# Performance work log

Measured on AMD Instinct MI355X. Metric: run time of the kernel, lower is better.

Reference implementation:

```python
import jax, jax.numpy as jnp
import numpy as np

N = 50000        # nodes
E = 1600000      # edges
IN = 256         # in_features
AD = 128         # attention_dim
H = 8            # heads
DK = AD // H     # per-head dim


def setup_inputs() -> dict:
    key = jax.random.key(0)
    ks = jax.random.split(key, 9)
    hi = jax.random.normal(ks[0], (N, IN), jnp.float32)
    radial = jax.random.uniform(ks[1], (E, 1), jnp.float32)
    edge = jax.random.randint(ks[2], (2, E), 0, N)
    # learned params (torch Linear: y = x @ W.T + b)
    Qw = jax.random.normal(ks[3], (AD, IN), jnp.float32) * 0.05
    Qb = jax.random.normal(ks[4], (AD,), jnp.float32) * 0.05
    Qrw = jax.random.normal(ks[5], (AD, 1), jnp.float32) * 0.05
    Qrb = jax.random.normal(ks[6], (AD,), jnp.float32) * 0.05
    Kw = jax.random.normal(ks[7], (AD, IN), jnp.float32) * 0.05
    Kb = jax.random.normal(ks[8], (AD,), jnp.float32) * 0.05
    return {"hi": hi, "radial": radial, "Qw": Qw, "Qb": Qb,
            "Qrw": Qrw, "Qrb": Qrb, "Kw": Kw, "Kb": Kb, "edge": edge}


def _segment_softmax(logits, seg, num_segments):
    # numerically stable softmax grouped by segment id (per head column)
    m = jax.ops.segment_max(logits, seg, num_segments=num_segments)  # [N, H]
    ex = jnp.exp(logits - m[seg])
    s = jax.ops.segment_sum(ex, seg, num_segments=num_segments)      # [N, H]
    return ex / s[seg]


def reference(hi, radial, Qw, Qb, Qrw, Qrb, Kw, Kb, edge):
    # node projections: [N, AD] -> [N, H, DK]
    q = (hi @ Qw.T + Qb).reshape(-1, H, DK)
    k = (hi @ Kw.T + Kb).reshape(-1, H, DK)
    # per-edge radial projection: [E, AD] -> [E, H, DK]
    q_rad = (radial @ Qrw.T + Qrb).reshape(-1, H, DK)
    # gather by edge endpoints; original transposes (1,2) then sums dim=1,
    # which is exactly a contraction over DK per head.
    src = q[edge[0]] + q_rad          # [E, H, DK]
    dst_k = k[edge[1]]                # [E, H, DK]
    prods = jnp.sum(src * dst_k, axis=-1) / np.sqrt(DK)  # [E, H]
    # square_plus=False, reweight_attention=False, attention_norm_idx=0
    attention = _segment_softmax(prods, edge[0], N)
    return attention, prods
```

## Files before the change

### kernel.cpp

```cpp
#include <hip/hip_runtime.h>
#include <hip/hip_fp16.h>
#include <math.h>

#define N_NODES 50000
#define EDGES   1600000
#define IN_F    256
#define AD      128
#define H       8
#define DK      16

typedef __attribute__((ext_vector_type(8))) _Float16 half8;
typedef __attribute__((ext_vector_type(4))) _Float16 half4;
typedef __attribute__((ext_vector_type(4))) float floatx4;

#ifndef __has_builtin
#define __has_builtin(x) 0
#endif

__global__ void wswz_kernel(const float* __restrict__ Qw,
                            const float* __restrict__ Kw,
                            half8* __restrict__ Wfrag) {
    const int idx = blockIdx.x * blockDim.x + threadIdx.x;
    if (idx >= 8 * 16 * 64) return;
    const int lane = idx & 63;
    const int nb   = (idx >> 6) & 15;
    const int kb   = idx >> 10;
    const int n    = nb * 16 + (lane & 15);
    const int k0   = kb * 32 + ((lane >> 4) << 3);
    const float* row = (n < AD) ? (Qw + (size_t)n * IN_F)
                                : (Kw + (size_t)(n - AD) * IN_F);
    half8 v;
#pragma unroll
    for (int j = 0; j < 8; j++) v[j] = (_Float16)row[k0 + j];
    Wfrag[idx] = v;
}

#define APAD 264
__global__ __launch_bounds__(256) void proj_mfma_kernel(
    const float* __restrict__ hi, const half8* __restrict__ Wfrag,
    const float* __restrict__ Qb, const float* __restrict__ Kb,
    __half* __restrict__ qh, __half* __restrict__ kh)
{
    __shared__ _Float16 Atile[64][APAD];
    const int r0 = blockIdx.x * 64;
    const int t  = threadIdx.x;

    {
        const int row = t >> 2;
        const int c4  = t & 3;
        const bool valid = (r0 + row) < N_NODES;
        const float4* src = (const float4*)(hi + (size_t)(r0 + row) * IN_F);
#pragma unroll
        for (int i = 0; i < 16; i++) {
            const int col4 = c4 + i * 4;
            float4 v = valid ? src[col4] : make_float4(0.f, 0.f, 0.f, 0.f);
            half4 hv;
            hv[0] = (_Float16)v.x; hv[1] = (_Float16)v.y;
            hv[2] = (_Float16)v.z; hv[3] = (_Float16)v.w;
            *(half4*)&Atile[row][col4 * 4] = hv;
        }
    }
    __syncthreads();

    const int wave = t >> 6;
    const int lane = t & 63;
    const int m    = lane & 15;
    const int quad = lane >> 4;

    floatx4 acc[4][4];
#pragma unroll
    for (int a = 0; a < 4; a++)
#pragma unroll
        for (int b = 0; b < 4; b++) acc[a][b] = (floatx4)0.f;

#pragma unroll
    for (int kb = 0; kb < 8; kb++) {
        half8 Af[4], Bf[4];
#pragma unroll
        for (int rb = 0; rb < 4; rb++)
            Af[rb] = *(const half8*)&Atile[rb * 16 + m][kb * 32 + quad * 8];
#pragma unroll
        for (int nbi = 0; nbi < 4; nbi++)
            Bf[nbi] = Wfrag[(size_t)(kb * 16 + wave * 4 + nbi) * 64 + lane];
#pragma unroll
        for (int rb = 0; rb < 4; rb++)
#pragma unroll
            for (int nbi = 0; nbi < 4; nbi++)
                acc[rb][nbi] = __builtin_amdgcn_mfma_f32_16x16x32_f16(
                    Af[rb], Bf[nbi], acc[rb][nbi], 0, 0, 0);
    }

#pragma unroll
    for (int nbi = 0; nbi < 4; nbi++) {
        const int n   = wave * 64 + nbi * 16 + m;
        const float bias = (n < AD) ? Qb[n] : Kb[n - AD];
        __half* out   = (n < AD) ? qh : kh;
        const int ncol = n & (AD - 1);
#pragma unroll
        for (int rb = 0; rb < 4; rb++) {
#pragma unroll
            for (int reg = 0; reg < 4; reg++) {
                const int row = r0 + rb * 16 + quad * 4 + reg;
                if (row < N_NODES)
                    out[(size_t)row * AD + ncol] = __float2half(acc[rb][nbi][reg] + bias);
            }
        }
    }
}

__global__ __launch_bounds__(256) void kprep_kernel(
    const __half* __restrict__ kh, const float* __restrict__ Qrw,
    const float* __restrict__ Qrb, float2* __restrict__ cb,
    float* __restrict__ ssum)
{
    const int t = blockIdx.x * blockDim.x + threadIdx.x;
    if (t >= N_NODES * H) return;
    ssum[t] = 0.0f;
    const int h = t & 7;
    const half8* kp = (const half8*)(kh + (size_t)(t >> 3) * AD + h * DK);
    half8 k0 = kp[0], k1 = kp[1];
    const float* rw = Qrw + h * DK;
    const float* rb = Qrb + h * DK;
    float brw = 0.f, crb = 0.f;
#pragma unroll
    for (int i = 0; i < 8; i++) {
        float kf = (float)k0[i];
        brw = fmaf(rw[i], kf, brw);
        crb = fmaf(rb[i], kf, crb);
    }
#pragma unroll
    for (int i = 0; i < 8; i++) {
        float kf = (float)k1[i];
        brw = fmaf(rw[8 + i], kf, brw);
        crb = fmaf(rb[8 + i], kf, crb);
    }
    cb[t] = make_float2(crb * 0.25f, brw * 0.25f);
}

__device__ __forceinline__ float dot16(half8 x0, half8 y0, half8 x1, half8 y1) {
#if __has_builtin(__builtin_amdgcn_fdot2)
    typedef _Float16 half2v __attribute__((ext_vector_type(2)));
    float acc = 0.f;
#pragma unroll
    for (int i = 0; i < 4; i++) {
        half2v a = {x0[2 * i], x0[2 * i + 1]};
        half2v b = {y0[2 * i], y0[2 * i + 1]};
        acc = __builtin_amdgcn_fdot2(a, b, acc, false);
    }
#pragma unroll
    for (int i = 0; i < 4; i++) {
        half2v a = {x1[2 * i], x1[2 * i + 1]};
        half2v b = {y1[2 * i], y1[2 * i + 1]};
        acc = __builtin_amdgcn_fdot2(a, b, acc, false);
    }
    return acc;
#else
    float acc = 0.f;
#pragma unroll
    for (int i = 0; i < 8; i++) acc += (float)x0[i] * (float)y0[i];
#pragma unroll
    for (int i = 0; i < 8; i++) acc += (float)x1[i] * (float)y1[i];
    return acc;
#endif
}

__global__ __launch_bounds__(256, 6) void edge_kernel(
    const __half* __restrict__ qh, const __half* __restrict__ kh,
    const float* __restrict__ radial, const int* __restrict__ edge,
    const float2* __restrict__ cb,
    float* __restrict__ prods, float* __restrict__ ssum)
{
    const int t = blockIdx.x * blockDim.x + threadIdx.x;
    const int e = t >> 3;
    const int h = t & 7;
    if (e >= EDGES / 2) return;
    const int eB = e + EDGES / 2;

    const int e0a = edge[e];
    const int e1a = edge[EDGES + e];
    const int e0b = edge[eB];
    const int e1b = edge[EDGES + eB];

    const half8* qpa = (const half8*)(qh + (size_t)e0a * AD + h * DK);
    const half8* kpa = (const half8*)(kh + (size_t)e1a * AD + h * DK);
    const half8* qpb = (const half8*)(qh + (size_t)e0b * AD + h * DK);
    const half8* kpb = (const half8*)(kh + (size_t)e1b * AD + h * DK);
    half8 qa0 = qpa[0], qa1 = qpa[1];
    half8 ka0 = kpa[0], ka1 = kpa[1];
    half8 qb0 = qpb[0], qb1 = qpb[1];
    half8 kb0 = kpb[0], kb1 = kpb[1];
    const float2 cba = cb[(size_t)e1a * H + h];
    const float2 cbb = cb[(size_t)e1b * H + h];
    const float ra = __builtin_nontemporal_load(&radial[e]);
    const float rb = __builtin_nontemporal_load(&radial[eB]);

    const float aa = dot16(qa0, ka0, qa1, ka1);
    const float ab = dot16(qb0, kb0, qb1, kb1);

    const float pa = fmaf(0.25f, aa, fmaf(ra, cba.y, cba.x));
    const float pb = fmaf(0.25f, ab, fmaf(rb, cbb.y, cbb.x));

    __builtin_nontemporal_store(pa, &prods[(size_t)e * H + h]);
    __builtin_nontemporal_store(pb, &prods[(size_t)eB * H + h]);

    atomicAdd(&ssum[e0a * H + h], __expf(pa));
    atomicAdd(&ssum[e0b * H + h], __expf(pb));
}

__global__ __launch_bounds__(256) void norm_kernel(
    const float* __restrict__ prods, const float* __restrict__ ssum,
    const int* __restrict__ edge, float* __restrict__ att)
{
    const int e = blockIdx.x * blockDim.x + threadIdx.x;
    if (e >= EDGES) return;
    const int e0 = edge[e];
    const floatx4* pp = (const floatx4*)(prods + (size_t)e * H);
    floatx4 p0 = __builtin_nontemporal_load(pp);
    floatx4 p1 = __builtin_nontemporal_load(pp + 1);
    const floatx4* sp = (const floatx4*)(ssum + (size_t)e0 * H);
    floatx4 s0 = sp[0], s1 = sp[1];
    floatx4 a0, a1;
#pragma unroll
    for (int i = 0; i < 4; i++) {
        a0[i] = __expf(p0[i]) / s0[i];
        a1[i] = __expf(p1[i]) / s1[i];
    }
    floatx4* ap = (floatx4*)(att + (size_t)e * H);
    __builtin_nontemporal_store(a0, ap);
    __builtin_nontemporal_store(a1, ap + 1);
}

extern "C" void kernel_launch(void* const* d_in, const int* in_sizes, int n_in,
                              void* d_out, int out_size, void* d_ws, size_t ws_size,
                              hipStream_t stream) {
    const float* hi     = (const float*)d_in[0];
    const float* radial = (const float*)d_in[1];
    const float* Qw     = (const float*)d_in[2];
    const float* Qb     = (const float*)d_in[3];
    const float* Qrw    = (const float*)d_in[4];
    const float* Qrb    = (const float*)d_in[5];
    const float* Kw     = (const float*)d_in[6];
    const float* Kb     = (const float*)d_in[7];
    const int*   edge   = (const int*)d_in[8];

    float* att   = (float*)d_out;
    float* prods = att + (size_t)EDGES * H;

    __half* qh   = (__half*)d_ws;
    __half* kh   = qh + (size_t)N_NODES * AD;
    float*  ssum = (float*)(kh + (size_t)N_NODES * AD);
    half8*  Wfrag = (half8*)(ssum + (size_t)N_NODES * H);
    float2* cbuf = (float2*)(Wfrag + 8 * 16 * 64);

    wswz_kernel<<<(8 * 16 * 64 + 255) / 256, 256, 0, stream>>>(Qw, Kw, Wfrag);
    proj_mfma_kernel<<<(N_NODES + 63) / 64, 256, 0, stream>>>(hi, Wfrag, Qb, Kb, qh, kh);
    kprep_kernel<<<(N_NODES * H + 255) / 256, 256, 0, stream>>>(kh, Qrw, Qrb, cbuf, ssum);
    edge_kernel<<<(EDGES * H / 2 + 255) / 256, 256, 0, stream>>>(qh, kh, radial, edge,
                                                                 cbuf, prods, ssum);
    norm_kernel<<<(EDGES + 255) / 256, 256, 0, stream>>>(prods, ssum, edge, att);
}
```

Measured before the change: 356.8 us.

## Fuse edge and normalize kernels via cooperative grid sync with register-held exponentials

Replaces the separate edge and norm kernels with one cooperative kernel. Each thread computes 49 edge-head logits, keeps their exponentials in registers, syncs the whole grid, then writes normalized attention without re-reading prods or recomputing exp. The aim is to remove the prods read-back and one kernel launch. In exchange it needs a grid-wide barrier, holds 49 floats per thread in registers (occupancy risk), uses less coalesced per-head indexing, and falls back to the old path if the cooperative launch fails. The fallback kernels also switch from nontemporal to ordinary loads and stores.

```diff
diff --git a/kernel.cpp b/kernel.cpp
--- a/kernel.cpp
+++ b/kernel.cpp
@@ -1,4 +1,5 @@
 #include <hip/hip_runtime.h>
+#include <hip/hip_cooperative_groups.h>
 #include <hip/hip_fp16.h>
 #include <math.h>
 
@@ -8,6 +9,12 @@
 #define AD      128
 #define H       8
 #define DK      16
+#define EH      (EDGES * H)
+
+#define FB   1024
+#define TPB  256
+#define TOT  (FB * TPB)
+#define UNITS 49
 
 typedef __attribute__((ext_vector_type(8))) _Float16 half8;
 typedef __attribute__((ext_vector_type(4))) _Float16 half4;
@@ -164,6 +171,58 @@
 #endif
 }
 
+__global__ __launch_bounds__(TPB, 4) void fused_edge_kernel(
+    const __half* __restrict__ qh, const __half* __restrict__ kh,
+    const float* __restrict__ radial, const int* __restrict__ edge,
+    const float2* __restrict__ cb,
+    float* __restrict__ prods, float* __restrict__ att,
+    float* __restrict__ ssum)
+{
+    const int tid = blockIdx.x * TPB + threadIdx.x;
+    float ex[UNITS];
+
+#pragma unroll
+    for (int u = 0; u < UNITS; u++) {
+        const int g = tid + u * TOT;
+        const bool act = (g < EH);
+        ex[u] = 0.f;
+        if (act) {
+            const int e = g >> 3;
+            const int h = g & 7;
+            const int e0 = edge[e];
+            const int e1 = edge[EDGES + e];
+            const half8* qp = (const half8*)(qh + (size_t)e0 * AD + h * DK);
+            const half8* kp = (const half8*)(kh + (size_t)e1 * AD + h * DK);
+            half8 q0 = qp[0], q1 = qp[1];
+            half8 k0 = kp[0], k1 = kp[1];
+            const float2 c = cb[e1 * H + h];
+            const float r = __builtin_nontemporal_load(&radial[e]);
+
+            const float a = dot16(q0, k0, q1, k1);
+            const float p = fmaf(0.25f, a, fmaf(r, c.y, c.x));
+            __builtin_nontemporal_store(p, &prods[g]);
+            const float exv = __expf(p);
+            ex[u] = exv;
+            atomicAdd(&ssum[e0 * H + h], exv);
+        }
+    }
+
+    cooperative_groups::this_grid().sync();
+
+#pragma unroll
+    for (int u = 0; u < UNITS; u++) {
+        const int g = tid + u * TOT;
+        if (g < EH) {
+            const int e = g >> 3;
+            const int h = g & 7;
+            const int e0 = edge[e];
+            const float s = ssum[e0 * H + h];
+            __builtin_nontemporal_store(ex[u] * __builtin_amdgcn_rcpf(s),
+                                        &att[g]);
+        }
+    }
+}
+
 __global__ __launch_bounds__(256, 6) void edge_kernel(
     const __half* __restrict__ qh, const __half* __restrict__ kh,
     const float* __restrict__ radial, const int* __restrict__ edge,
@@ -191,8 +250,8 @@
     half8 kb0 = kpb[0], kb1 = kpb[1];
     const float2 cba = cb[(size_t)e1a * H + h];
     const float2 cbb = cb[(size_t)e1b * H + h];
-    const float ra = __builtin_nontemporal_load(&radial[e]);
-    const float rb = __builtin_nontemporal_load(&radial[eB]);
+    const float ra = radial[e];
+    const float rb = radial[eB];
 
     const float aa = dot16(qa0, ka0, qa1, ka1);
     const float ab = dot16(qb0, kb0, qb1, kb1);
@@ -200,8 +259,8 @@
     const float pa = fmaf(0.25f, aa, fmaf(ra, cba.y, cba.x));
     const float pb = fmaf(0.25f, ab, fmaf(rb, cbb.y, cbb.x));
 
-    __builtin_nontemporal_store(pa, &prods[(size_t)e * H + h]);
-    __builtin_nontemporal_store(pb, &prods[(size_t)eB * H + h]);
+    prods[(size_t)e * H + h]  = pa;
+    prods[(size_t)eB * H + h] = pb;
 
     atomicAdd(&ssum[e0a * H + h], __expf(pa));
     atomicAdd(&ssum[e0b * H + h], __expf(pb));
@@ -215,8 +274,8 @@
     if (e >= EDGES) return;
     const int e0 = edge[e];
     const floatx4* pp = (const floatx4*)(prods + (size_t)e * H);
-    floatx4 p0 = __builtin_nontemporal_load(pp);
-    floatx4 p1 = __builtin_nontemporal_load(pp + 1);
+    floatx4 p0 = pp[0];
+    floatx4 p1 = pp[1];
     const floatx4* sp = (const floatx4*)(ssum + (size_t)e0 * H);
     floatx4 s0 = sp[0], s1 = sp[1];
     floatx4 a0, a1;
@@ -255,7 +314,20 @@
     wswz_kernel<<<(8 * 16 * 64 + 255) / 256, 256, 0, stream>>>(Qw, Kw, Wfrag);
     proj_mfma_kernel<<<(N_NODES + 63) / 64, 256, 0, stream>>>(hi, Wfrag, Qb, Kb, qh, kh);
     kprep_kernel<<<(N_NODES * H + 255) / 256, 256, 0, stream>>>(kh, Qrw, Qrb, cbuf, ssum);
-    edge_kernel<<<(EDGES * H / 2 + 255) / 256, 256, 0, stream>>>(qh, kh, radial, edge,
-                                                                 cbuf, prods, ssum);
-    norm_kernel<<<(EDGES + 255) / 256, 256, 0, stream>>>(prods, ssum, edge, att);
-}
+
+    {
+        const __half* qh_c = qh; const __half* kh_c = kh;
+        const float2* cb_c = cbuf;
+        void* args[] = { (void*)&qh_c, (void*)&kh_c, (void*)&radial,
+                         (void*)&edge, (void*)&cb_c, (void*)&prods,
+                         (void*)&att, (void*)&ssum };
+        hipError_t st = hipLaunchCooperativeKernel(
+            (const void*)fused_edge_kernel, dim3(FB), dim3(TPB), args, 0, stream);
+        if (st != hipSuccess) {
+            edge_kernel<<<(EDGES * H / 2 + 255) / 256, 256, 0, stream>>>(
+                qh, kh, radial, edge, cbuf, prods, ssum);
+            norm_kernel<<<(EDGES + 255) / 256, 256, 0, stream>>>(
+                prods, ssum, edge, att);
+        }
+    }
+}
```

New measurement: 630.1 us. 1.77x slower.

## Switch node features, sums and prods to head-major layout for edge gathers

Applied to the files above, without the earlier changes.

Stores q/k projections, softmax sums and the K-side bias terms in head-major layout ([H][N][16]), so each edge-kernel block handles one head. The per-head working set (q,k,cb,ssum for one head) becomes much smaller and can stay in cache during random gathers. Prods are first written head-major to a workspace buffer, and the norm kernel transposes them back into the output while also replacing the division with a reciprocal. The cost is an extra prods write and read, strided reads in the norm kernel, and edge indices that are now read once per head instead of once per edge.

```diff
diff --git a/kernel.cpp b/kernel.cpp
--- a/kernel.cpp
+++ b/kernel.cpp
@@ -8,10 +8,14 @@
 #define AD      128
 #define H       8
 #define DK      16
+#define EH      (EDGES * H)
+#define EPB     512
+#define BPH     (EDGES / EPB)
 
 typedef __attribute__((ext_vector_type(8))) _Float16 half8;
 typedef __attribute__((ext_vector_type(4))) _Float16 half4;
 typedef __attribute__((ext_vector_type(4))) float floatx4;
+typedef __attribute__((ext_vector_type(2))) float floatx2;
 
 #ifndef __has_builtin
 #define __has_builtin(x) 0
@@ -96,13 +100,16 @@
         const float bias = (n < AD) ? Qb[n] : Kb[n - AD];
         __half* out   = (n < AD) ? qh : kh;
         const int ncol = n & (AD - 1);
+        const int hh   = ncol >> 4;
+        const int d    = ncol & 15;
 #pragma unroll
         for (int rb = 0; rb < 4; rb++) {
 #pragma unroll
             for (int reg = 0; reg < 4; reg++) {
                 const int row = r0 + rb * 16 + quad * 4 + reg;
                 if (row < N_NODES)
-                    out[(size_t)row * AD + ncol] = __float2half(acc[rb][nbi][reg] + bias);
+                    out[((size_t)hh * N_NODES + row) * 16 + d] =
+                        __float2half(acc[rb][nbi][reg] + bias);
             }
         }
     }
@@ -113,11 +120,12 @@
     const float* __restrict__ Qrb, float2* __restrict__ cb,
     float* __restrict__ ssum)
 {
-    const int t = blockIdx.x * blockDim.x + threadIdx.x;
-    if (t >= N_NODES * H) return;
-    ssum[t] = 0.0f;
-    const int h = t & 7;
-    const half8* kp = (const half8*)(kh + (size_t)(t >> 3) * AD + h * DK);
+    const int n = blockIdx.x * blockDim.x + threadIdx.x;
+    const int h = blockIdx.y;
+    if (n >= N_NODES) return;
+    const size_t idx = (size_t)h * N_NODES + n;
+    ssum[idx] = 0.0f;
+    const half8* kp = (const half8*)(kh + idx * 16);
     half8 k0 = kp[0], k1 = kp[1];
     const float* rw = Qrw + h * DK;
     const float* rb = Qrb + h * DK;
@@ -134,7 +142,7 @@
         brw = fmaf(rw[8 + i], kf, brw);
         crb = fmaf(rb[8 + i], kf, crb);
     }
-    cb[t] = make_float2(crb * 0.25f, brw * 0.25f);
+    cb[idx] = make_float2(crb * 0.25f, brw * 0.25f);
 }
 
 __device__ __forceinline__ float dot16(half8 x0, half8 y0, half8 x1, half8 y1) {
@@ -164,35 +172,36 @@
 #endif
 }
 
-__global__ __launch_bounds__(256, 6) void edge_kernel(
+__global__ __launch_bounds__(256) void edge_kernel(
     const __half* __restrict__ qh, const __half* __restrict__ kh,
     const float* __restrict__ radial, const int* __restrict__ edge,
     const float2* __restrict__ cb,
-    float* __restrict__ prods, float* __restrict__ ssum)
-{
-    const int t = blockIdx.x * blockDim.x + threadIdx.x;
-    const int e = t >> 3;
-    const int h = t & 7;
-    if (e >= EDGES / 2) return;
-    const int eB = e + EDGES / 2;
-
-    const int e0a = edge[e];
-    const int e1a = edge[EDGES + e];
-    const int e0b = edge[eB];
-    const int e1b = edge[EDGES + eB];
-
-    const half8* qpa = (const half8*)(qh + (size_t)e0a * AD + h * DK);
-    const half8* kpa = (const half8*)(kh + (size_t)e1a * AD + h * DK);
-    const half8* qpb = (const half8*)(qh + (size_t)e0b * AD + h * DK);
-    const half8* kpb = (const half8*)(kh + (size_t)e1b * AD + h * DK);
+    float* __restrict__ prods_hm, float* __restrict__ ssum)
+{
+    const int h     = blockIdx.x & 7;
+    const int chunk = blockIdx.x >> 3;
+    const size_t hb = (size_t)h * N_NODES;
+
+    const int eA = chunk * EPB + threadIdx.x;
+    const int eB = eA + 256;
+
+    const int e0a = __builtin_nontemporal_load(&edge[eA]);
+    const int e1a = __builtin_nontemporal_load(&edge[EDGES + eA]);
+    const int e0b = __builtin_nontemporal_load(&edge[eB]);
+    const int e1b = __builtin_nontemporal_load(&edge[EDGES + eB]);
+    const float ra = __builtin_nontemporal_load(&radial[eA]);
+    const float rb = __builtin_nontemporal_load(&radial[eB]);
+
+    const half8* qpa = (const half8*)(qh + (hb + e0a) * 16);
+    const half8* kpa = (const half8*)(kh + (hb + e1a) * 16);
+    const half8* qpb = (const half8*)(qh + (hb + e0b) * 16);
+    const half8* kpb = (const half8*)(kh + (hb + e1b) * 16);
     half8 qa0 = qpa[0], qa1 = qpa[1];
     half8 ka0 = kpa[0], ka1 = kpa[1];
     half8 qb0 = qpb[0], qb1 = qpb[1];
     half8 kb0 = kpb[0], kb1 = kpb[1];
-    const float2 cba = cb[(size_t)e1a * H + h];
-    const float2 cbb = cb[(size_t)e1b * H + h];
-    const float ra = __builtin_nontemporal_load(&radial[e]);
-    const float rb = __builtin_nontemporal_load(&radial[eB]);
+    const floatx2 cba = ((const floatx2*)cb)[hb + e1a];
+    const floatx2 cbb = ((const floatx2*)cb)[hb + e1b];
 
     const float aa = dot16(qa0, ka0, qa1, ka1);
     const float ab = dot16(qb0, kb0, qb1, kb1);
@@ -200,31 +209,41 @@
     const float pa = fmaf(0.25f, aa, fmaf(ra, cba.y, cba.x));
     const float pb = fmaf(0.25f, ab, fmaf(rb, cbb.y, cbb.x));
 
-    __builtin_nontemporal_store(pa, &prods[(size_t)e * H + h]);
-    __builtin_nontemporal_store(pb, &prods[(size_t)eB * H + h]);
-
-    atomicAdd(&ssum[e0a * H + h], __expf(pa));
-    atomicAdd(&ssum[e0b * H + h], __expf(pb));
+    __builtin_nontemporal_store(pa, &prods_hm[(size_t)h * EDGES + eA]);
+    __builtin_nontemporal_store(pb, &prods_hm[(size_t)h * EDGES + eB]);
+
+    atomicAdd(&ssum[hb + e0a], __expf(pa));
+    atomicAdd(&ssum[hb + e0b], __expf(pb));
 }
 
 __global__ __launch_bounds__(256) void norm_kernel(
-    const float* __restrict__ prods, const float* __restrict__ ssum,
-    const int* __restrict__ edge, float* __restrict__ att)
+    const float* __restrict__ prods_hm, const float* __restrict__ ssum,
+    const int* __restrict__ edge, float* __restrict__ att,
+    float* __restrict__ prods_out)
 {
     const int e = blockIdx.x * blockDim.x + threadIdx.x;
     if (e >= EDGES) return;
     const int e0 = edge[e];
-    const floatx4* pp = (const floatx4*)(prods + (size_t)e * H);
-    floatx4 p0 = __builtin_nontemporal_load(pp);
-    floatx4 p1 = __builtin_nontemporal_load(pp + 1);
-    const floatx4* sp = (const floatx4*)(ssum + (size_t)e0 * H);
-    floatx4 s0 = sp[0], s1 = sp[1];
-    floatx4 a0, a1;
-#pragma unroll
-    for (int i = 0; i < 4; i++) {
-        a0[i] = __expf(p0[i]) / s0[i];
-        a1[i] = __expf(p1[i]) / s1[i];
-    }
+
+    floatx4 p0, p1, a0, a1;
+#pragma unroll
+    for (int h = 0; h < 4; h++)
+        p0[h] = __builtin_nontemporal_load(&prods_hm[(size_t)h * EDGES + e]);
+#pragma unroll
+    for (int h = 0; h < 4; h++)
+        p1[h] = __builtin_nontemporal_load(&prods_hm[(size_t)(h + 4) * EDGES + e]);
+
+#pragma unroll
+    for (int h = 0; h < 4; h++) {
+        const float s0 = ssum[(size_t)h * N_NODES + e0];
+        const float s1 = ssum[(size_t)(h + 4) * N_NODES + e0];
+        a0[h] = __expf(p0[h]) * __builtin_amdgcn_rcpf(s0);
+        a1[h] = __expf(p1[h]) * __builtin_amdgcn_rcpf(s1);
+    }
+
+    floatx4* pp = (floatx4*)(prods_out + (size_t)e * H);
+    __builtin_nontemporal_store(p0, pp);
+    __builtin_nontemporal_store(p1, pp + 1);
     floatx4* ap = (floatx4*)(att + (size_t)e * H);
     __builtin_nontemporal_store(a0, ap);
     __builtin_nontemporal_store(a1, ap + 1);
@@ -247,15 +266,18 @@
     float* prods = att + (size_t)EDGES * H;
 
     __half* qh   = (__half*)d_ws;
-    __half* kh   = qh + (size_t)N_NODES * AD;
-    float*  ssum = (float*)(kh + (size_t)N_NODES * AD);
-    half8*  Wfrag = (half8*)(ssum + (size_t)N_NODES * H);
+    __half* kh   = qh + (size_t)H * N_NODES * 16;
+    float*  ssum = (float*)(kh + (size_t)H * N_NODES * 16);
+    half8*  Wfrag = (half8*)(ssum + (size_t)H * N_NODES);
     float2* cbuf = (float2*)(Wfrag + 8 * 16 * 64);
+    float*  prods_hm = (float*)(cbuf + (size_t)H * N_NODES);
 
     wswz_kernel<<<(8 * 16 * 64 + 255) / 256, 256, 0, stream>>>(Qw, Kw, Wfrag);
     proj_mfma_kernel<<<(N_NODES + 63) / 64, 256, 0, stream>>>(hi, Wfrag, Qb, Kb, qh, kh);
-    kprep_kernel<<<(N_NODES * H + 255) / 256, 256, 0, stream>>>(kh, Qrw, Qrb, cbuf, ssum);
-    edge_kernel<<<(EDGES * H / 2 + 255) / 256, 256, 0, stream>>>(qh, kh, radial, edge,
-                                                                 cbuf, prods, ssum);
-    norm_kernel<<<(EDGES + 255) / 256, 256, 0, stream>>>(prods, ssum, edge, att);
-}
+    kprep_kernel<<<dim3((N_NODES + 255) / 256, H), 256, 0, stream>>>(
+        kh, Qrw, Qrb, cbuf, ssum);
+    edge_kernel<<<BPH * H, 256, 0, stream>>>(qh, kh, radial, edge,
+                                             cbuf, prods_hm, ssum);
+    norm_kernel<<<(EDGES + 255) / 256, 256, 0, stream>>>(prods_hm, ssum, edge,
+                                                         att, prods);
+}
```

Result: slower. 902.2 us (+152.9%).
